# Performance work log

Hardware: AMD Instinct MI355X
Metric: run time of the kernel (lower is better)

Reference implementation:

```python
import jax, jax.numpy as jnp
import numpy as np

S, H = 8192, 2048

def setup_inputs() -> dict:
    key = jax.random.key(0)
    k1, k2, k3 = jax.random.split(key, 3)
    hidden = jax.random.normal(k1, (1, H), dtype=jnp.float32)
    encoder_outputs = jax.random.normal(k2, (S, 1, H), dtype=jnp.float32)
    W = jax.random.normal(k3, (H, H), dtype=jnp.float32) * (1.0 / np.sqrt(H))
    b = jnp.zeros((H,), dtype=jnp.float32)
    return {"hidden": hidden, "encoder_outputs": encoder_outputs, "W": W, "b": b}

def reference(hidden, encoder_outputs, W, b):
    # hidden: [1, H] -> [H]; encoder_outputs: [S, 1, H] -> [S, H]
    h = hidden[0]                      # [H]
    enc = encoder_outputs[:, 0, :]     # [S, H]
    # method='general': energy_i = h . (W @ enc_i + b)
    proj = jnp.einsum('sh,kh->sk', enc, W) + b   # [S, H] (Linear: x @ W.T + b)
    energies = proj @ h                          # [S]
    attn = jax.nn.softmax(energies, axis=0)      # softmax over seq dim
    return attn[None, None, :]                   # [1, 1, S]
```

## Files before the change

kernel.cpp:

```cpp
#include <hip/hip_runtime.h>


#define Hdim 2048
#define Sdim 8192
#define KCHUNKS 32
#define KROWS 64

__global__ void k1_partial(const float* __restrict__ W, const float* __restrict__ hid,
                           float* __restrict__ part) {
    int t = threadIdx.x;
    int colBase = blockIdx.x * 1024 + t * 4;
    int k0 = blockIdx.y * KROWS;
    float4 acc = {0.f, 0.f, 0.f, 0.f};
    for (int i = 0; i < KROWS; ++i) {
        int k = k0 + i;
        float hk = hid[k];
        float4 w = *reinterpret_cast<const float4*>(W + (size_t)k * Hdim + colBase);
        acc.x += w.x * hk;
        acc.y += w.y * hk;
        acc.z += w.z * hk;
        acc.w += w.w * hk;
    }
    *reinterpret_cast<float4*>(part + (size_t)blockIdx.y * Hdim + colBase) = acc;
}

__global__ void k1b_reduce(const float* __restrict__ part, const float* __restrict__ b,
                           const float* __restrict__ hid, float* __restrict__ v,
                           float* __restrict__ c) {
    if (blockIdx.x < 8) {
        int h = blockIdx.x * 256 + threadIdx.x;
        float s = 0.f;
#pragma unroll
        for (int j = 0; j < KCHUNKS; ++j) s += part[j * Hdim + h];
        v[h] = s;
    } else {
        __shared__ float red[256];
        float s = 0.f;
        for (int k = threadIdx.x; k < Hdim; k += 256) s += b[k] * hid[k];
        red[threadIdx.x] = s;
        __syncthreads();
        for (int off = 128; off > 0; off >>= 1) {
            if (threadIdx.x < off) red[threadIdx.x] += red[threadIdx.x + off];
            __syncthreads();
        }
        if (threadIdx.x == 0) *c = red[0];
    }
}

__global__ void k2_energies(const float* __restrict__ enc, const float* __restrict__ v,
                            const float* __restrict__ c, float* __restrict__ e) {
    int wave = threadIdx.x >> 6;
    int lane = threadIdx.x & 63;
    int s = blockIdx.x * 4 + wave;
    const float* row = enc + (size_t)s * Hdim;
    float acc = 0.f;
#pragma unroll
    for (int i = 0; i < 8; ++i) {
        int idx = i * 256 + lane * 4;
        float4 a = *reinterpret_cast<const float4*>(row + idx);
        float4 w = *reinterpret_cast<const float4*>(v + idx);
        acc += a.x * w.x + a.y * w.y + a.z * w.z + a.w * w.w;
    }
#pragma unroll
    for (int off = 32; off > 0; off >>= 1) acc += __shfl_xor(acc, off, 64);
    if (lane == 0) e[s] = acc + *c;
}

__global__ void k3_softmax(const float* __restrict__ e, float* __restrict__ out) {
    __shared__ float red[16];
    __shared__ float bcast;
    int t = threadIdx.x;
    int lane = t & 63, wid = t >> 6;
    float4 a = *reinterpret_cast<const float4*>(e + t * 8);
    float4 bq = *reinterpret_cast<const float4*>(e + t * 8 + 4);
    float vals[8] = {a.x, a.y, a.z, a.w, bq.x, bq.y, bq.z, bq.w};
    float m = vals[0];
#pragma unroll
    for (int i = 1; i < 8; ++i) m = fmaxf(m, vals[i]);
#pragma unroll
    for (int off = 32; off > 0; off >>= 1) m = fmaxf(m, __shfl_xor(m, off, 64));
    if (lane == 0) red[wid] = m;
    __syncthreads();
    if (wid == 0) {
        float mm = (lane < 16) ? red[lane] : -1e30f;
#pragma unroll
        for (int off = 8; off > 0; off >>= 1) mm = fmaxf(mm, __shfl_xor(mm, off, 64));
        if (lane == 0) bcast = mm;
    }
    __syncthreads();
    m = bcast;
    float ex[8];
    float s = 0.f;
#pragma unroll
    for (int i = 0; i < 8; ++i) {
        ex[i] = __expf(vals[i] - m);
        s += ex[i];
    }
#pragma unroll
    for (int off = 32; off > 0; off >>= 1) s += __shfl_xor(s, off, 64);
    __syncthreads();
    if (lane == 0) red[wid] = s;
    __syncthreads();
    if (wid == 0) {
        float ss = (lane < 16) ? red[lane] : 0.f;
#pragma unroll
        for (int off = 8; off > 0; off >>= 1) ss += __shfl_xor(ss, off, 64);
        if (lane == 0) bcast = ss;
    }
    __syncthreads();
    float inv = 1.0f / bcast;
    float4 o1 = {ex[0] * inv, ex[1] * inv, ex[2] * inv, ex[3] * inv};
    float4 o2 = {ex[4] * inv, ex[5] * inv, ex[6] * inv, ex[7] * inv};
    *reinterpret_cast<float4*>(out + t * 8) = o1;
    *reinterpret_cast<float4*>(out + t * 8 + 4) = o2;
}

extern "C" void kernel_launch(void* const* d_in, const int* in_sizes, int n_in,
                              void* d_out, int out_size, void* d_ws, size_t ws_size,
                              hipStream_t stream) {
    const float* hid = (const float*)d_in[0];
    const float* enc = (const float*)d_in[1];
    const float* W   = (const float*)d_in[2];
    const float* b   = (const float*)d_in[3];
    float* out = (float*)d_out;
    float* ws = (float*)d_ws;

    float* part = ws;
    float* v    = part + KCHUNKS * Hdim;
    float* e    = v + Hdim;
    float* c    = e + Sdim;

    k1_partial<<<dim3(2, KCHUNKS), 256, 0, stream>>>(W, hid, part);
    k1b_reduce<<<9, 256, 0, stream>>>(part, b, hid, v, c);
    k2_energies<<<Sdim / 4, 256, 0, stream>>>(enc, v, c, e);
    k3_softmax<<<1, 1024, 0, stream>>>(e, out);
}
```

Baseline: 28.99 us.

## Split W-vector GEMV across more blocks and drop softmax-invariant bias term

Increases the number of K-chunks in the W^T·h partial GEMV from 32 to 128 so the 16MB W read uses many more workgroups. The reduction kernel is reorganised to sum 128 partials per column across 32 blocks using shared memory. The b·h constant is removed since softmax is invariant to a uniform shift, eliminating the bias dot product and its load in the energy kernel. The cost is a larger partial buffer written and re-read.

```diff
diff --git a/kernel.cpp b/kernel.cpp
--- a/kernel.cpp
+++ b/kernel.cpp
@@ -3,16 +3,17 @@
 
 #define Hdim 2048
 #define Sdim 8192
-#define KCHUNKS 32
-#define KROWS 64
+#define PCHUNKS 128
+#define PROWS 16
 
 __global__ void k1_partial(const float* __restrict__ W, const float* __restrict__ hid,
                            float* __restrict__ part) {
     int t = threadIdx.x;
     int colBase = blockIdx.x * 1024 + t * 4;
-    int k0 = blockIdx.y * KROWS;
+    int k0 = blockIdx.y * PROWS;
     float4 acc = {0.f, 0.f, 0.f, 0.f};
-    for (int i = 0; i < KROWS; ++i) {
+#pragma unroll
+    for (int i = 0; i < PROWS; ++i) {
         int k = k0 + i;
         float hk = hid[k];
         float4 w = *reinterpret_cast<const float4*>(W + (size_t)k * Hdim + colBase);
@@ -24,34 +25,24 @@
     *reinterpret_cast<float4*>(part + (size_t)blockIdx.y * Hdim + colBase) = acc;
 }
 
-__global__ void k1b_reduce(const float* __restrict__ part, const float* __restrict__ b,
-                           const float* __restrict__ hid, float* __restrict__ v,
-                           float* __restrict__ c) {
-    if (blockIdx.x < 8) {
-        int h = blockIdx.x * 256 + threadIdx.x;
-        float s = 0.f;
+__global__ void k1b_reduce(const float* __restrict__ part, float* __restrict__ v) {
+    __shared__ float red[256];
+    int t = threadIdx.x;
+    int col = blockIdx.x * 64 + (t & 63);
+    int j0 = (t >> 6) * 32;
+    float s = 0.f;
 #pragma unroll
-        for (int j = 0; j < KCHUNKS; ++j) s += part[j * Hdim + h];
-        v[h] = s;
-    } else {
-        __shared__ float red[256];
-        float s = 0.f;
-        for (int k = threadIdx.x; k < Hdim; k += 256) s += b[k] * hid[k];
-        red[threadIdx.x] = s;
-        __syncthreads();
-        for (int off = 128; off > 0; off >>= 1) {
-            if (threadIdx.x < off) red[threadIdx.x] += red[threadIdx.x + off];
-            __syncthreads();
-        }
-        if (threadIdx.x == 0) *c = red[0];
-    }
+    for (int j = 0; j < 32; ++j) s += part[(size_t)(j0 + j) * Hdim + col];
+    red[t] = s;
+    __syncthreads();
+    if (t < 64) v[col] = red[t] + red[64 + t] + red[128 + t] + red[192 + t];
 }
 
 __global__ void k2_energies(const float* __restrict__ enc, const float* __restrict__ v,
-                            const float* __restrict__ c, float* __restrict__ e) {
-    int wave = threadIdx.x >> 6;
-    int lane = threadIdx.x & 63;
-    int s = blockIdx.x * 4 + wave;
+                            float* __restrict__ e) {
+    int t = threadIdx.x;
+    int lane = t & 63;
+    int s = blockIdx.x * 4 + (t >> 6);
     const float* row = enc + (size_t)s * Hdim;
     float acc = 0.f;
 #pragma unroll
@@ -63,7 +54,7 @@
     }
 #pragma unroll
     for (int off = 32; off > 0; off >>= 1) acc += __shfl_xor(acc, off, 64);
-    if (lane == 0) e[s] = acc + *c;
+    if (lane == 0) e[s] = acc;
 }
 
 __global__ void k3_softmax(const float* __restrict__ e, float* __restrict__ out) {
@@ -121,17 +112,15 @@
     const float* hid = (const float*)d_in[0];
     const float* enc = (const float*)d_in[1];
     const float* W   = (const float*)d_in[2];
-    const float* b   = (const float*)d_in[3];
     float* out = (float*)d_out;
     float* ws = (float*)d_ws;
 
     float* part = ws;
-    float* v    = part + KCHUNKS * Hdim;
+    float* v    = part + PCHUNKS * Hdim;
     float* e    = v + Hdim;
-    float* c    = e + Sdim;
 
-    k1_partial<<<dim3(2, KCHUNKS), 256, 0, stream>>>(W, hid, part);
-    k1b_reduce<<<9, 256, 0, stream>>>(part, b, hid, v, c);
-    k2_energies<<<Sdim / 4, 256, 0, stream>>>(enc, v, c, e);
+    k1_partial<<<dim3(2, PCHUNKS), 256, 0, stream>>>(W, hid, part);
+    k1b_reduce<<<32, 256, 0, stream>>>(part, v);
+    k2_energies<<<Sdim / 4, 256, 0, stream>>>(enc, v, e);
     k3_softmax<<<1, 1024, 0, stream>>>(e, out);
 }
```

Measured after the change: 26.52 us. 8.5% less time.
